# Optimization experiments

Measured on AMD Instinct MI355X. Metric: run time of the kernel, lower is better.

## Reference

```python
import jax, jax.numpy as jnp
import numpy as np

N = 50000      # num nodes
E = 800000     # num edges (before self loops)
F_IN = 128     # fea_size
D = 128        # g_dim_per_layer[i]
H = 4          # heads
C = D // H     # out_channels per head
NEG_SLOPE = 0.2  # PyG GATConv default leaky_relu slope


def setup_inputs() -> dict:
    key = jax.random.key(0)
    ks = jax.random.split(key, 20)
    inp = {
        "x": jax.random.normal(ks[0], (N, F_IN), dtype=jnp.float32),
        "edge_index": jax.random.randint(ks[1], (2, E), 0, N, dtype=jnp.int32),
        "w0": jax.random.normal(ks[2], (F_IN, D), dtype=jnp.float32) * 0.05,
        "b0": jnp.zeros((D,), dtype=jnp.float32),
    }
    for i in (1, 2, 3):
        k = 4 * i
        inp[f"w{i}"] = jax.random.normal(ks[k], (D, D), dtype=jnp.float32) * 0.05
        inp[f"a_src{i}"] = jax.random.normal(ks[k + 1], (H, C), dtype=jnp.float32) * 0.1
        inp[f"a_dst{i}"] = jax.random.normal(ks[k + 2], (H, C), dtype=jnp.float32) * 0.1
        inp[f"b{i}"] = jnp.zeros((D,), dtype=jnp.float32)
    return inp


def _gat_layer(x, src, dst, w, a_src, a_dst, b):
    # PyG GATConv (eval mode, dropout inactive, add_self_loops already applied)
    n = x.shape[0]
    xp = (x @ w).reshape(n, H, C)                       # [N,H,C]
    al_s = jnp.einsum("nhc,hc->nh", xp, a_src)          # [N,H]
    al_d = jnp.einsum("nhc,hc->nh", xp, a_dst)          # [N,H]
    e = jax.nn.leaky_relu(al_s[src] + al_d[dst], NEG_SLOPE)  # [E',H]
    # softmax over incoming edges of each destination node
    m = jax.ops.segment_max(e, dst, num_segments=n)
    e = jnp.exp(e - m[dst])
    s = jax.ops.segment_sum(e, dst, num_segments=n)
    alpha = e / s[dst]                                  # [E',H]
    msg = alpha[:, :, None] * xp[src]                   # [E',H,C]
    out = jax.ops.segment_sum(msg, dst, num_segments=n)  # [N,H,C]
    return out.reshape(n, H * C) + b


def reference(x, edge_index, w0, b0, w1, a_src1, a_dst1, b1,
              w2, a_src2, a_dst2, b2, w3, a_src3, a_dst3, b3):
    n = x.shape[0]
    loops = jnp.arange(n, dtype=edge_index.dtype)
    ei = jnp.concatenate([edge_index, jnp.stack([loops, loops])], axis=1)
    src, dst = ei[0], ei[1]  # messages flow src -> dst (PyG convention)

    h = x @ w0 + b0
    h = jax.nn.relu(h + _gat_layer(h, src, dst, w1, a_src1, a_dst1, b1))
    h = jax.nn.relu(h + _gat_layer(h, src, dst, w2, a_src2, a_dst2, b2))
    return _gat_layer(h, src, dst, w3, a_src3, a_dst3, b3)
```

## Files before the change

### kernel.cpp

```cpp
#include <hip/hip_runtime.h>

#define F 128
#define HEADS 4
#define NEG 0.2f
#define CAP 64
#define CAPP 68
#define CB 6144

typedef unsigned short u16;
typedef unsigned int u32;
typedef __attribute__((ext_vector_type(8))) unsigned short us8;
typedef __attribute__((ext_vector_type(8))) short short8;
typedef __attribute__((ext_vector_type(4))) float f32x4;

__device__ __forceinline__ float bf2f(u16 u) {
  union { u32 i; float f; } v; v.i = ((u32)u) << 16; return v.f;
}
__device__ __forceinline__ float bflo(u32 p) {
  union { u32 i; float f; } v; v.i = p << 16; return v.f;
}
__device__ __forceinline__ float bfhi(u32 p) {
  union { u32 i; float f; } v; v.i = p & 0xFFFF0000u; return v.f;
}
__device__ __forceinline__ u16 f2bf(float f) {
  union { u32 i; float f; } v; v.f = f;
  if (((v.i >> 23) & 0xFF) == 0xFF) return 0;
  u32 r = v.i + 0x7FFF + ((v.i >> 16) & 1);
  return (u16)(r >> 16);
}
__device__ __forceinline__ float sane(float f) {
  union { u32 i; float f; } v; v.f = f;
  return (((v.i >> 23) & 0xFF) == 0xFF) ? 0.f : f;
}
__device__ __forceinline__ u16 bfsane(u16 u) {
  return (((u >> 7) & 0xFF) == 0xFF) ? (u16)0 : u;
}

__device__ __forceinline__ bool detect_f32_wave(const u16* __restrict__ p) {
  int lane = threadIdx.x & 63;
  const us8* q = (const us8*)p + lane * 4;
  int c = 0;
  #pragma unroll
  for (int k = 0; k < 4; k++) {
    us8 v = q[k];
    #pragma unroll
    for (int j = 0; j < 8; j++) { unsigned e = (v[j] >> 7) & 0xFF; c += (e >= 0xF8); }
  }
  #pragma unroll
  for (int off = 32; off; off >>= 1) c += __shfl_xor(c, off);
  return c > 4;
}

__global__ __launch_bounds__(256) void fill_const_bf16(u16* __restrict__ p, u16 v, int n) {
  int i = blockIdx.x * blockDim.x + threadIdx.x;
  if (i < n) p[i] = v;
}

__global__ __launch_bounds__(256) void setup(
    const void* w0, const void* w1, const void* w2, const void* w3,
    const void* b0, const void* b1, const void* b2, const void* b3,
    const void* as1, const void* ad1, const void* as2, const void* ad2,
    const void* as3, const void* ad3,
    u16* __restrict__ wsz, u16* __restrict__ avf, float* __restrict__ par,
    int* __restrict__ flg, int* __restrict__ gcur) {
  __shared__ float vv[8][128];
  bool f32 = detect_f32_wave((const u16*)w0);
  int blk = blockIdx.x, tid = threadIdx.x;
  if (blk < 32) {
    int idx = blk * 256 + tid;
    int layer = idx >> 11;
    int rest  = idx & 2047;
    int lane = rest & 63;
    int ts   = rest >> 6;
    int s = ts & 3, t = ts >> 2;
    int kbase = s * 32 + (lane >> 4) * 8;
    int nn    = t * 16 + (lane & 15);
    const void* W = (layer == 0) ? w0 : (layer == 1) ? w1 : (layer == 2) ? w2 : w3;
    us8 o;
    #pragma unroll
    for (int j = 0; j < 8; j++) {
      int off = (kbase + j) * F + nn;
      o[j] = f32 ? f2bf(sane(((const float*)W)[off])) : bfsane(((const u16*)W)[off]);
    }
    *(us8*)(wsz + (size_t)idx * 8) = o;
  } else if (blk < 37) {
    int t = (blk - 32) * 256 + tid;
    if (t < 1280) {
      const void* tab[10] = {b0, b1, b2, b3, as1, ad1, as2, ad2, as3, ad3};
      const void* src = tab[t >> 7];
      int idx = t & 127;
      float v = f32 ? ((const float*)src)[idx] : bf2f(((const u16*)src)[idx]);
      par[t] = sane(v);
    }
  } else if (blk == 37) {
    gcur[tid] = 0;
    if (tid == 0) flg[0] = f32 ? 1 : 0;
  } else {
    int l = blk - 38;
    const void* W   = (l == 0) ? w1 : (l == 1) ? w2 : w3;
    const void* asp = (l == 0) ? as1 : (l == 1) ? as2 : as3;
    const void* adp = (l == 0) ? ad1 : (l == 1) ? ad2 : ad3;
    for (int e = tid; e < 1024; e += 256) {
      int vec = e >> 7, k = e & 127;
      int h = vec & 3;
      const void* av = (vec < 4) ? asp : adp;
      float sum = 0.f;
      for (int c = 0; c < 32; c++) {
        int col = h * 32 + c;
        float wv_ = f32 ? ((const float*)W)[k * F + col] : bf2f(((const u16*)W)[k * F + col]);
        float aa  = f32 ? ((const float*)av)[col]        : bf2f(((const u16*)av)[col]);
        sum += sane(wv_) * sane(aa);
      }
      vv[vec][k] = sane(sum);
    }
    __syncthreads();
    int s = tid >> 6, lane = tid & 63;
    int quad = lane >> 4, l15 = lane & 15;
    int kbase = s * 32 + quad * 8;
    us8 o;
    #pragma unroll
    for (int j = 0; j < 8; j++)
      o[j] = (l15 < 8) ? f2bf(vv[l15][kbase + j]) : (u16)0;
    *(us8*)(avf + (((size_t)l * 4 + s) * 64 + lane) * 8) = o;
  }
}

__device__ __forceinline__ void gemm_tile(
    int m0, int lane, const void* __restrict__ A, int f32in,
    const u16* __restrict__ wszL, const float* __restrict__ biasc,
    const u16* __restrict__ avfL, u16* __restrict__ Cm,
    float* __restrict__ al_s, float* __restrict__ al_d, int nrows) {
  int quad = lane >> 4, l15 = lane & 15;
  int mrow = m0 + l15;
  int ml = mrow < nrows ? mrow : (nrows - 1);
  short8 af[4];
  if (f32in) {
    const float* ar = (const float*)A + (size_t)ml * F;
    #pragma unroll
    for (int s = 0; s < 4; s++) {
      float4 u = *(const float4*)(ar + s * 32 + quad * 8);
      float4 v = *(const float4*)(ar + s * 32 + quad * 8 + 4);
      short8 p;
      p[0] = (short)f2bf(sane(u.x)); p[1] = (short)f2bf(sane(u.y));
      p[2] = (short)f2bf(sane(u.z)); p[3] = (short)f2bf(sane(u.w));
      p[4] = (short)f2bf(sane(v.x)); p[5] = (short)f2bf(sane(v.y));
      p[6] = (short)f2bf(sane(v.z)); p[7] = (short)f2bf(sane(v.w));
      af[s] = p;
    }
  } else {
    const u16* ar = (const u16*)A + (size_t)ml * F;
    #pragma unroll
    for (int s = 0; s < 4; s++) af[s] = *(const short8*)(ar + s * 32 + quad * 8);
  }

  f32x4 acc[8];
  #pragma unroll
  for (int t = 0; t < 8; t++) acc[t] = (f32x4){0.f, 0.f, 0.f, 0.f};
  f32x4 accL = (f32x4){0.f, 0.f, 0.f, 0.f};

  #pragma unroll
  for (int s = 0; s < 4; s++) {
    short8 bfr[8];
    #pragma unroll
    for (int t = 0; t < 8; t++)
      bfr[t] = *(const short8*)(wszL + (size_t)(((t << 2) | s) * 64 + lane) * 8);
    if (avfL) {
      short8 av = *(const short8*)(avfL + (size_t)(s * 64 + lane) * 8);
      accL = __builtin_amdgcn_mfma_f32_16x16x32_bf16(af[s], av, accL, 0, 0, 0);
    }
    #pragma unroll
    for (int t = 0; t < 8; t++)
      acc[t] = __builtin_amdgcn_mfma_f32_16x16x32_bf16(af[s], bfr[t], acc[t], 0, 0, 0);
  }

  #pragma unroll
  for (int t = 0; t < 8; t++) {
    int cc = t * 16 + l15;
    float b = biasc ? biasc[cc] : 0.f;
    #pragma unroll
    for (int r = 0; r < 4; r++) {
      int row = m0 + quad * 4 + r;
      if (row < nrows) Cm[(size_t)row * F + cc] = f2bf(sane(acc[t][r] + b));
    }
  }
  if (avfL && l15 < 8) {
    float* dst = (l15 < 4) ? al_s : al_d;
    int h = l15 & 3;
    #pragma unroll
    for (int r = 0; r < 4; r++) {
      int row = m0 + quad * 4 + r;
      if (row < nrows) dst[(size_t)row * 4 + h] = sane(accL[r]);
    }
  }
}

__device__ __forceinline__ void scatter_body(const int* __restrict__ ei,
                                             int* __restrict__ gcur,
                                             int2* __restrict__ ebuf,
                                             int E, int E2, int n, int blk) {
  __shared__ int lcnt[256];
  __shared__ int gbase[256];
  int tid = threadIdx.x;
  lcnt[tid] = 0;
  __syncthreads();
  int srcv[16], dstv[16], rnk[16];
  #pragma unroll
  for (int i = 0; i < 16; i++) {
    int e = blk * 4096 + i * 256 + tid;
    rnk[i] = -1;
    if (e < E2) {
      int src, dst;
      if (e < E) { src = ei[e]; dst = ei[E + e]; }
      else       { src = dst = e - E; }
      if ((unsigned)dst < (unsigned)n) {
        srcv[i] = src; dstv[i] = dst;
        rnk[i] = atomicAdd(&lcnt[dst >> 8], 1);
      }
    }
  }
  __syncthreads();
  int c = lcnt[tid];
  gbase[tid] = c ? atomicAdd(&gcur[tid], c) : 0;
  __syncthreads();
  #pragma unroll
  for (int i = 0; i < 16; i++) {
    if (rnk[i] >= 0) {
      int b = dstv[i] >> 8;
      int slot = gbase[b] + rnk[i];
      if (slot < CB) ebuf[(size_t)b * CB + slot] = make_int2(srcv[i], dstv[i]);
    }
  }
}

__device__ __forceinline__ void fill_body(const int* __restrict__ gcur,
                                          const int2* __restrict__ ebuf,
                                          int* __restrict__ rp,
                                          int* __restrict__ col, int n, int b) {
  __shared__ int sc[256];
  __shared__ int ncnt[256];
  __shared__ int nofs[256];
  __shared__ int wsums[4];
  __shared__ int total_s;
  int tid = threadIdx.x, lane = tid & 63, wv = tid >> 6;
  int v = min(gcur[tid], CB);
  int x = v;
  #pragma unroll
  for (int off = 1; off < 64; off <<= 1) {
    int t = __shfl_up(x, off);
    if (lane >= off) x += t;
  }
  if (lane == 63) wsums[wv] = x;
  __syncthreads();
  int add = 0;
  for (int w = 0; w < wv; w++) add += wsums[w];
  sc[tid] = add + x - v;
  if (tid == 255) total_s = add + x;
  __syncthreads();
  int tot = min(gcur[b], CB);
  int colbase = sc[b];
  const int2* eb = ebuf + (size_t)b * CB;
  ncnt[tid] = 0;
  __syncthreads();
  for (int j = tid; j < tot; j += 256) atomicAdd(&ncnt[eb[j].y & 255], 1);
  __syncthreads();
  v = ncnt[tid];
  x = v;
  #pragma unroll
  for (int off = 1; off < 64; off <<= 1) {
    int t = __shfl_up(x, off);
    if (lane >= off) x += t;
  }
  if (lane == 63) wsums[wv] = x;
  __syncthreads();
  add = 0;
  for (int w = 0; w < wv; w++) add += wsums[w];
  nofs[tid] = add + x - v;
  int node = (b << 8) + tid;
  if (node < n) rp[node] = colbase + nofs[tid];
  if (b == 0 && tid == 0) rp[n] = total_s;
  __syncthreads();
  ncnt[tid] = 0;
  __syncthreads();
  for (int j = tid; j < tot; j += 256) {
    int2 e = eb[j];
    int ln = e.y & 255;
    int r = atomicAdd(&ncnt[ln], 1);
    col[colbase + nofs[ln] + r] = e.x;
  }
}

__global__ __launch_bounds__(256) void scatter_gemm0(
    const int* __restrict__ ei, int* __restrict__ gcur, int2* __restrict__ ebuf,
    int E, int E2, int n, int SB,
    const void* __restrict__ x, const int* __restrict__ flg,
    const u16* __restrict__ wsz, const float* __restrict__ b0c,
    u16* __restrict__ hio) {
  int blk = blockIdx.x;
  if (blk < SB) {
    scatter_body(ei, gcur, ebuf, E, E2, n, blk);
  } else {
    int tid = threadIdx.x, wv = tid >> 6, lane = tid & 63;
    int m0 = (blk - SB) * 64 + wv * 16;
    gemm_tile(m0, lane, x, flg[0], wsz, b0c, nullptr, hio, nullptr, nullptr, n);
  }
}

__global__ __launch_bounds__(256) void fill_gemm1(
    const int* __restrict__ gcur, const int2* __restrict__ ebuf,
    int* __restrict__ rp, int* __restrict__ col, int n, int NBv,
    const void* __restrict__ hA, const u16* __restrict__ wszL,
    const u16* __restrict__ avfL, u16* __restrict__ xp,
    float* __restrict__ al_s, float* __restrict__ al_d) {
  int blk = blockIdx.x;
  if (blk < NBv) {
    fill_body(gcur, ebuf, rp, col, n, blk);
  } else {
    int tid = threadIdx.x, wv = tid >> 6, lane = tid & 63;
    int m0 = (blk - NBv) * 64 + wv * 16;
    gemm_tile(m0, lane, hA, 0, wszL, nullptr, avfL, xp, al_s, al_d, n);
  }
}

__global__ __launch_bounds__(128) void gemm_std(
    const void* __restrict__ A, const u16* __restrict__ wszL,
    const u16* __restrict__ avfL, u16* __restrict__ Cm,
    float* __restrict__ al_s, float* __restrict__ al_d, int nrows) {
  int tid = threadIdx.x, wv = tid >> 6, lane = tid & 63;
  int m0 = blockIdx.x * 32 + wv * 16;
  gemm_tile(m0, lane, A, 0, wszL, nullptr, avfL, Cm, al_s, al_d, nrows);
}

#define ACC8(w_, P_)                                    \
  a0 += (w_) * bflo((P_).x); a1 += (w_) * bfhi((P_).x); \
  a2 += (w_) * bflo((P_).y); a3 += (w_) * bfhi((P_).y); \
  a4 += (w_) * bflo((P_).z); a5 += (w_) * bfhi((P_).z); \
  a6 += (w_) * bflo((P_).w); a7 += (w_) * bfhi((P_).w);

__global__ __launch_bounds__(256) void gat_aggregate(
    const u16* __restrict__ xp, const float* __restrict__ al_s,
    const float* __restrict__ al_d, const int* __restrict__ row_ptr,
    const int* __restrict__ col, const float* __restrict__ biasc,
    u16* __restrict__ hio, const int* __restrict__ flgp,
    int n, int E2, int mode) {
  __shared__ int   sb[4][4][CAP];
  __shared__ float wb[4][4][4][CAPP];
  int tid = threadIdx.x;
  int wv = tid >> 6, lane = tid & 63;
  int q = lane >> 4, g = lane & 15;
  int node = blockIdx.x * 16 + wv * 4 + q;
  bool active = node < n;
  int beg = 0, end = 0;
  float ald_[4] = {0.f, 0.f, 0.f, 0.f};
  if (active) {
    beg = row_ptr[node]; end = row_ptr[node + 1];
    if (beg < 0) beg = 0; if (beg > E2) beg = E2;
    if (end < beg) end = beg; if (end > E2) end = E2;
    float4 qd = ((const float4*)al_d)[node];
    ald_[0] = qd.x; ald_[1] = qd.y; ald_[2] = qd.z; ald_[3] = qd.w;
  }
  int deg = end - beg;
  int ch = g * 8, head = g >> 2;
  u32 cb = (u32)g * 16;
  const char* xpb = (const char*)xp;
  float a0 = 0.f, a1 = 0.f, a2 = 0.f, a3 = 0.f;
  float a4 = 0.f, a5 = 0.f, a6 = 0.f, a7 = 0.f;
  float inv;

  if (deg <= CAP) {
    float er[4][4];
    float m4[4] = {-1e30f, -1e30f, -1e30f, -1e30f};
    #pragma unroll
    for (int it = 0; it < 4; it++) {
      int jj = g + it * 16;
      if (jj < deg) {
        int src = col[beg + jj];
        if ((unsigned)src >= (unsigned)n) src = node;
        sb[wv][q][jj] = src;
        float4 qs = ((const float4*)al_s)[src];
        float as_[4] = {qs.x, qs.y, qs.z, qs.w};
        #pragma unroll
        for (int h = 0; h < 4; h++) {
          float e = as_[h] + ald_[h];
          e = (e > 0.f) ? e : NEG * e;
          er[it][h] = e;
          m4[h] = fmaxf(m4[h], e);
        }
      }
    }
    #pragma unroll
    for (int off = 8; off; off >>= 1)
      #pragma unroll
      for (int h = 0; h < 4; h++) m4[h] = fmaxf(m4[h], __shfl_xor(m4[h], off));
    float s4[4] = {0.f, 0.f, 0.f, 0.f};
    #pragma unroll
    for (int it = 0; it < 4; it++) {
      int jj = g + it * 16;
      if (jj < deg) {
        #pragma unroll
        for (int h = 0; h < 4; h++) {
          float w = __expf(er[it][h] - m4[h]);
          s4[h] += w;
          wb[wv][q][h][jj] = w;
        }
      }
    }
    #pragma unroll
    for (int off = 8; off; off >>= 1)
      #pragma unroll
      for (int h = 0; h < 4; h++) s4[h] += __shfl_xor(s4[h], off);
    inv = (s4[head] > 0.f) ? 1.f / s4[head] : 0.f;
    __asm__ volatile("s_waitcnt lgkmcnt(0)" ::: "memory");
    const int* srow = sb[wv][q];
    const float* wrow = wb[wv][q][head];
    int j = 0;
    if (deg >= 4) {
      int4 sa = *(const int4*)(srow);
      float4 wa = *(const float4*)(wrow);
      uint4 P0 = *(const uint4*)(xpb + (((u32)sa.x << 8) + cb));
      uint4 P1 = *(const uint4*)(xpb + (((u32)sa.y << 8) + cb));
      uint4 P2 = *(const uint4*)(xpb + (((u32)sa.z << 8) + cb));
      uint4 P3 = *(const uint4*)(xpb + (((u32)sa.w << 8) + cb));
      for (; j + 8 <= deg; j += 4) {
        int4 sn = *(const int4*)(srow + j + 4);
        float4 wn = *(const float4*)(wrow + j + 4);
        uint4 Q0 = *(const uint4*)(xpb + (((u32)sn.x << 8) + cb));
        uint4 Q1 = *(const uint4*)(xpb + (((u32)sn.y << 8) + cb));
        uint4 Q2 = *(const uint4*)(xpb + (((u32)sn.z << 8) + cb));
        uint4 Q3 = *(const uint4*)(xpb + (((u32)sn.w << 8) + cb));
        ACC8(wa.x, P0); ACC8(wa.y, P1); ACC8(wa.z, P2); ACC8(wa.w, P3);
        wa = wn; P0 = Q0; P1 = Q1; P2 = Q2; P3 = Q3;
      }
      ACC8(wa.x, P0); ACC8(wa.y, P1); ACC8(wa.z, P2); ACC8(wa.w, P3);
      j += 4;
    }
    for (; j < deg; j++) {
      int s0 = srow[j];
      float w0 = wrow[j];
      uint4 p0 = *(const uint4*)(xpb + (((u32)s0 << 8) + cb));
      ACC8(w0, p0);
    }
    a0 *= inv; a1 *= inv; a2 *= inv; a3 *= inv;
    a4 *= inv; a5 *= inv; a6 *= inv; a7 *= inv;
  } else {
    float m = -1.0e30f, s = 0.f;
    for (int j = beg; j < end; ++j) {
      int src = col[j];
      if ((unsigned)src >= (unsigned)n) continue;
      float e = al_s[src * 4 + head] + ald_[head];
      e = (e > 0.f) ? e : NEG * e;
      float mn = fmaxf(m, e);
      float scale = __expf(m - mn);
      float w = __expf(e - mn);
      uint4 pv = *(const uint4*)(xpb + (((u32)src << 8) + cb));
      s = s * scale + w;
      a0 = a0 * scale + w * bflo(pv.x); a1 = a1 * scale + w * bfhi(pv.x);
      a2 = a2 * scale + w * bflo(pv.y); a3 = a3 * scale + w * bfhi(pv.y);
      a4 = a4 * scale + w * bflo(pv.z); a5 = a5 * scale + w * bfhi(pv.z);
      a6 = a6 * scale + w * bflo(pv.w); a7 = a7 * scale + w * bfhi(pv.w);
      m = mn;
    }
    inv = (s > 0.f) ? 1.f / s : 0.f;
    a0 *= inv; a1 *= inv; a2 *= inv; a3 *= inv;
    a4 *= inv; a5 *= inv; a6 *= inv; a7 *= inv;
  }

  if (!active) return;
  float4 b4a = *(const float4*)(biasc + ch);
  float4 b4b = *(const float4*)(biasc + ch + 4);
  float o0 = sane(a0) + b4a.x, o1 = sane(a1) + b4a.y;
  float o2 = sane(a2) + b4a.z, o3 = sane(a3) + b4a.w;
  float o4 = sane(a4) + b4b.x, o5 = sane(a5) + b4b.y;
  float o6 = sane(a6) + b4b.z, o7 = sane(a7) + b4b.w;
  size_t o = (size_t)node * F + ch;
  if (mode == 0) {
    uint4 hv = *(const uint4*)(hio + o);
    o0 = fmaxf(bflo(hv.x) + o0, 0.f);
    o1 = fmaxf(bfhi(hv.x) + o1, 0.f);
    o2 = fmaxf(bflo(hv.y) + o2, 0.f);
    o3 = fmaxf(bfhi(hv.y) + o3, 0.f);
    o4 = fmaxf(bflo(hv.z) + o4, 0.f);
    o5 = fmaxf(bfhi(hv.z) + o5, 0.f);
    o6 = fmaxf(bflo(hv.w) + o6, 0.f);
    o7 = fmaxf(bfhi(hv.w) + o7, 0.f);
    uint4 st;
    st.x = ((u32)f2bf(sane(o1)) << 16) | (u32)f2bf(sane(o0));
    st.y = ((u32)f2bf(sane(o3)) << 16) | (u32)f2bf(sane(o2));
    st.z = ((u32)f2bf(sane(o5)) << 16) | (u32)f2bf(sane(o4));
    st.w = ((u32)f2bf(sane(o7)) << 16) | (u32)f2bf(sane(o6));
    *(uint4*)(hio + o) = st;
  } else {
    if (flgp[0]) {
      float4 s1 = {sane(o0), sane(o1), sane(o2), sane(o3)};
      float4 s2 = {sane(o4), sane(o5), sane(o6), sane(o7)};
      *(float4*)((float*)hio + o) = s1;
      *(float4*)((float*)hio + o + 4) = s2;
    } else {
      uint4 st;
      st.x = ((u32)f2bf(sane(o1)) << 16) | (u32)f2bf(sane(o0));
      st.y = ((u32)f2bf(sane(o3)) << 16) | (u32)f2bf(sane(o2));
      st.z = ((u32)f2bf(sane(o5)) << 16) | (u32)f2bf(sane(o4));
      st.w = ((u32)f2bf(sane(o7)) << 16) | (u32)f2bf(sane(o6));
      *(uint4*)(hio + o) = st;
    }
  }
}

extern "C" void kernel_launch(void* const* d_in, const int* in_sizes, int n_in,
                              void* d_out, int out_size, void* d_ws, size_t ws_size,
                              hipStream_t stream) {
  const int* ei = (const int*)d_in[1];

  const int N  = in_sizes[0] / F;
  const int E  = in_sizes[1] / 2;
  const int E2 = E + N;
  const int NB = (N + 255) >> 8;
  const int SB = (E2 + 4095) / 4096;
  const int GB64  = (N + 63) / 64;
  const int GB128 = (N + 31) / 32;
  const int AGGB  = (N + 15) / 16;

  uintptr_t base = ((uintptr_t)d_ws + 255) & ~(uintptr_t)255;
  size_t off_par = 0;
  size_t off_flg = off_par + (size_t)1536 * 4;
  size_t off_wsz = off_flg + 256;
  size_t off_avf = off_wsz + (size_t)65536 * 2;
  size_t off_xp  = off_avf + (size_t)6144 * 2;
  size_t off_als = off_xp  + (size_t)N * F * 2;
  size_t off_ald = off_als + (size_t)N * HEADS * 4;
  size_t off_gc  = off_ald + (size_t)N * HEADS * 4;
  size_t off_rp  = off_gc  + 1024;
  size_t off_col = off_rp  + (size_t)(N + 1) * 4;
  size_t off_eb  = (off_col + (size_t)E2 * 4 + 255) & ~(size_t)255;
  size_t need    = off_eb + (size_t)NB * CB * 8 + 512 + ((uintptr_t)d_ws & 255);

  if (ws_size < need) {
    fill_const_bf16<<<(out_size + 255) / 256, 256, 0, stream>>>(
        (u16*)d_out, (u16)0x4316, out_size);
    return;
  }

  float* par   = (float*)(base + off_par);
  int* flg     = (int*)(base + off_flg);
  u16* wsz     = (u16*)(base + off_wsz);
  u16* avf     = (u16*)(base + off_avf);
  u16* xp      = (u16*)(base + off_xp);
  float* al_s  = (float*)(base + off_als);
  float* al_d  = (float*)(base + off_ald);
  int* gcur    = (int*)(base + off_gc);
  int* row_ptr = (int*)(base + off_rp);
  int* col     = (int*)(base + off_col);
  int2* ebuf   = (int2*)(base + off_eb);

  float* bc[4];
  for (int l = 0; l < 4; ++l) bc[l] = par + (size_t)l * 128;

  u16* hio = (u16*)d_out;

  setup<<<41, 256, 0, stream>>>(
      d_in[2], d_in[4], d_in[8], d_in[12],
      d_in[3], d_in[7], d_in[11], d_in[15],
      d_in[5], d_in[6], d_in[9], d_in[10], d_in[13], d_in[14],
      wsz, avf, par, flg, gcur);

  scatter_gemm0<<<SB + GB64, 256, 0, stream>>>(
      ei, gcur, ebuf, E, E2, N, SB, d_in[0], flg, wsz, bc[0], hio);

  fill_gemm1<<<NB + GB64, 256, 0, stream>>>(
      gcur, ebuf, row_ptr, col, N, NB,
      hio, wsz + (size_t)1 * 16384, avf, xp, al_s, al_d);

  gat_aggregate<<<AGGB, 256, 0, stream>>>(
      xp, al_s, al_d, row_ptr, col, bc[1], hio, flg, N, E2, 0);
  gemm_std<<<GB128, 128, 0, stream>>>(hio, wsz + (size_t)2 * 16384,
                                      avf + (size_t)1 * 2048, xp, al_s, al_d, N);
  gat_aggregate<<<AGGB, 256, 0, stream>>>(
      xp, al_s, al_d, row_ptr, col, bc[2], hio, flg, N, E2, 0);
  gemm_std<<<GB128, 128, 0, stream>>>(hio, wsz + (size_t)3 * 16384,
                                      avf + (size_t)2 * 2048, xp, al_s, al_d, N);
  gat_aggregate<<<AGGB, 256, 0, stream>>>(
      xp, al_s, al_d, row_ptr, col, bc[3], hio, flg, N, E2, 1);
}
```

Before: 296.4 us.

## Fuse next-layer GEMM into GAT aggregation kernel with ping-pong buffers

The separate gemm_std launches are removed. Each aggregation block now stages its 16 output rows in shared memory and immediately runs the next layer's MFMA projection and attention-logit products on them. Ping-pong xp/al buffers are added so the fused GEMM can write while other blocks still read the previous projection. This saves two launches and a reread of h, but adds a block-wide sync, extra weight loads per block and more workspace memory.

```diff
diff --git a/kernel.cpp b/kernel.cpp
--- a/kernel.cpp
+++ b/kernel.cpp
@@ -6,6 +6,7 @@
 #define CAP 64
 #define CAPP 68
 #define CB 6144
+#define HTS 136
 
 typedef unsigned short u16;
 typedef unsigned int u32;
@@ -321,29 +322,23 @@
   }
 }
 
-__global__ __launch_bounds__(128) void gemm_std(
-    const void* __restrict__ A, const u16* __restrict__ wszL,
-    const u16* __restrict__ avfL, u16* __restrict__ Cm,
-    float* __restrict__ al_s, float* __restrict__ al_d, int nrows) {
-  int tid = threadIdx.x, wv = tid >> 6, lane = tid & 63;
-  int m0 = blockIdx.x * 32 + wv * 16;
-  gemm_tile(m0, lane, A, 0, wszL, nullptr, avfL, Cm, al_s, al_d, nrows);
-}
-
 #define ACC8(w_, P_)                                    \
   a0 += (w_) * bflo((P_).x); a1 += (w_) * bfhi((P_).x); \
   a2 += (w_) * bflo((P_).y); a3 += (w_) * bfhi((P_).y); \
   a4 += (w_) * bflo((P_).z); a5 += (w_) * bfhi((P_).z); \
   a6 += (w_) * bflo((P_).w); a7 += (w_) * bfhi((P_).w);
 
-__global__ __launch_bounds__(256) void gat_aggregate(
+__global__ __launch_bounds__(256) void gat_agg_gemm(
     const u16* __restrict__ xp, const float* __restrict__ al_s,
     const float* __restrict__ al_d, const int* __restrict__ row_ptr,
     const int* __restrict__ col, const float* __restrict__ biasc,
     u16* __restrict__ hio, const int* __restrict__ flgp,
-    int n, int E2, int mode) {
+    int n, int E2, int mode,
+    const u16* __restrict__ wszL, const u16* __restrict__ avfL,
+    u16* __restrict__ xpo, float* __restrict__ also_, float* __restrict__ aldo) {
   __shared__ int   sb[4][4][CAP];
   __shared__ float wb[4][4][4][CAPP];
+  __shared__ u16   ht[16 * HTS];
   int tid = threadIdx.x;
   int wv = tid >> 6, lane = tid & 63;
   int q = lane >> 4, g = lane & 15;
@@ -464,31 +459,83 @@
     a4 *= inv; a5 *= inv; a6 *= inv; a7 *= inv;
   }
 
-  if (!active) return;
-  float4 b4a = *(const float4*)(biasc + ch);
-  float4 b4b = *(const float4*)(biasc + ch + 4);
-  float o0 = sane(a0) + b4a.x, o1 = sane(a1) + b4a.y;
-  float o2 = sane(a2) + b4a.z, o3 = sane(a3) + b4a.w;
-  float o4 = sane(a4) + b4b.x, o5 = sane(a5) + b4b.y;
-  float o6 = sane(a6) + b4b.z, o7 = sane(a7) + b4b.w;
-  size_t o = (size_t)node * F + ch;
   if (mode == 0) {
-    uint4 hv = *(const uint4*)(hio + o);
-    o0 = fmaxf(bflo(hv.x) + o0, 0.f);
-    o1 = fmaxf(bfhi(hv.x) + o1, 0.f);
-    o2 = fmaxf(bflo(hv.y) + o2, 0.f);
-    o3 = fmaxf(bfhi(hv.y) + o3, 0.f);
-    o4 = fmaxf(bflo(hv.z) + o4, 0.f);
-    o5 = fmaxf(bfhi(hv.z) + o5, 0.f);
-    o6 = fmaxf(bflo(hv.w) + o6, 0.f);
-    o7 = fmaxf(bfhi(hv.w) + o7, 0.f);
-    uint4 st;
-    st.x = ((u32)f2bf(sane(o1)) << 16) | (u32)f2bf(sane(o0));
-    st.y = ((u32)f2bf(sane(o3)) << 16) | (u32)f2bf(sane(o2));
-    st.z = ((u32)f2bf(sane(o5)) << 16) | (u32)f2bf(sane(o4));
-    st.w = ((u32)f2bf(sane(o7)) << 16) | (u32)f2bf(sane(o6));
-    *(uint4*)(hio + o) = st;
+    uint4 st = make_uint4(0u, 0u, 0u, 0u);
+    if (active) {
+      float4 b4a = *(const float4*)(biasc + ch);
+      float4 b4b = *(const float4*)(biasc + ch + 4);
+      float o0 = sane(a0) + b4a.x, o1 = sane(a1) + b4a.y;
+      float o2 = sane(a2) + b4a.z, o3 = sane(a3) + b4a.w;
+      float o4 = sane(a4) + b4b.x, o5 = sane(a5) + b4b.y;
+      float o6 = sane(a6) + b4b.z, o7 = sane(a7) + b4b.w;
+      size_t o = (size_t)node * F + ch;
+      uint4 hv = *(const uint4*)(hio + o);
+      o0 = fmaxf(bflo(hv.x) + o0, 0.f);
+      o1 = fmaxf(bfhi(hv.x) + o1, 0.f);
+      o2 = fmaxf(bflo(hv.y) + o2, 0.f);
+      o3 = fmaxf(bfhi(hv.y) + o3, 0.f);
+      o4 = fmaxf(bflo(hv.z) + o4, 0.f);
+      o5 = fmaxf(bfhi(hv.z) + o5, 0.f);
+      o6 = fmaxf(bflo(hv.w) + o6, 0.f);
+      o7 = fmaxf(bfhi(hv.w) + o7, 0.f);
+      st.x = ((u32)f2bf(sane(o1)) << 16) | (u32)f2bf(sane(o0));
+      st.y = ((u32)f2bf(sane(o3)) << 16) | (u32)f2bf(sane(o2));
+      st.z = ((u32)f2bf(sane(o5)) << 16) | (u32)f2bf(sane(o4));
+      st.w = ((u32)f2bf(sane(o7)) << 16) | (u32)f2bf(sane(o6));
+      *(uint4*)(hio + o) = st;
+    }
+    *(uint4*)&ht[(wv * 4 + q) * HTS + ch] = st;
+    __syncthreads();
+
+    int quad = lane >> 4, l15 = lane & 15;
+    short8 af[4];
+    #pragma unroll
+    for (int s = 0; s < 4; s++)
+      af[s] = *(const short8*)&ht[l15 * HTS + s * 32 + quad * 8];
+    f32x4 acc0 = (f32x4){0.f, 0.f, 0.f, 0.f};
+    f32x4 acc1 = (f32x4){0.f, 0.f, 0.f, 0.f};
+    f32x4 accL = (f32x4){0.f, 0.f, 0.f, 0.f};
+    int t0 = wv * 2;
+    #pragma unroll
+    for (int s = 0; s < 4; s++) {
+      short8 bv0 = *(const short8*)(wszL + (size_t)(((t0 << 2) | s) * 64 + lane) * 8);
+      short8 bv1 = *(const short8*)(wszL + (size_t)((((t0 + 1) << 2) | s) * 64 + lane) * 8);
+      if (wv == 0) {
+        short8 av = *(const short8*)(avfL + (size_t)(s * 64 + lane) * 8);
+        accL = __builtin_amdgcn_mfma_f32_16x16x32_bf16(af[s], av, accL, 0, 0, 0);
+      }
+      acc0 = __builtin_amdgcn_mfma_f32_16x16x32_bf16(af[s], bv0, acc0, 0, 0, 0);
+      acc1 = __builtin_amdgcn_mfma_f32_16x16x32_bf16(af[s], bv1, acc1, 0, 0, 0);
+    }
+    int row0 = blockIdx.x * 16;
+    #pragma unroll
+    for (int tt = 0; tt < 2; tt++) {
+      f32x4 ac = tt ? acc1 : acc0;
+      int cc = (t0 + tt) * 16 + l15;
+      #pragma unroll
+      for (int r = 0; r < 4; r++) {
+        int row = row0 + quad * 4 + r;
+        if (row < n) xpo[(size_t)row * F + cc] = f2bf(sane(ac[r]));
+      }
+    }
+    if (wv == 0 && l15 < 8) {
+      float* dst = (l15 < 4) ? also_ : aldo;
+      int h = l15 & 3;
+      #pragma unroll
+      for (int r = 0; r < 4; r++) {
+        int row = row0 + quad * 4 + r;
+        if (row < n) dst[(size_t)row * 4 + h] = sane(accL[r]);
+      }
+    }
   } else {
+    if (!active) return;
+    float4 b4a = *(const float4*)(biasc + ch);
+    float4 b4b = *(const float4*)(biasc + ch + 4);
+    float o0 = sane(a0) + b4a.x, o1 = sane(a1) + b4a.y;
+    float o2 = sane(a2) + b4a.z, o3 = sane(a3) + b4a.w;
+    float o4 = sane(a4) + b4b.x, o5 = sane(a5) + b4b.y;
+    float o6 = sane(a6) + b4b.z, o7 = sane(a7) + b4b.w;
+    size_t o = (size_t)node * F + ch;
     if (flgp[0]) {
       float4 s1 = {sane(o0), sane(o1), sane(o2), sane(o3)};
       float4 s2 = {sane(o4), sane(o5), sane(o6), sane(o7)};
@@ -516,7 +563,6 @@
   const int NB = (N + 255) >> 8;
   const int SB = (E2 + 4095) / 4096;
   const int GB64  = (N + 63) / 64;
-  const int GB128 = (N + 31) / 32;
   const int AGGB  = (N + 15) / 16;
 
   uintptr_t base = ((uintptr_t)d_ws + 255) & ~(uintptr_t)255;
@@ -531,7 +577,10 @@
   size_t off_rp  = off_gc  + 1024;
   size_t off_col = off_rp  + (size_t)(N + 1) * 4;
   size_t off_eb  = (off_col + (size_t)E2 * 4 + 255) & ~(size_t)255;
-  size_t need    = off_eb + (size_t)NB * CB * 8 + 512 + ((uintptr_t)d_ws & 255);
+  size_t off_xp2 = (off_eb + (size_t)NB * CB * 8 + 255) & ~(size_t)255;
+  size_t off_als2 = off_xp2 + (size_t)N * F * 2;
+  size_t off_ald2 = off_als2 + (size_t)N * HEADS * 4;
+  size_t need    = off_ald2 + (size_t)N * HEADS * 4 + 512 + ((uintptr_t)d_ws & 255);
 
   if (ws_size < need) {
     fill_const_bf16<<<(out_size + 255) / 256, 256, 0, stream>>>(
@@ -543,13 +592,16 @@
   int* flg     = (int*)(base + off_flg);
   u16* wsz     = (u16*)(base + off_wsz);
   u16* avf     = (u16*)(base + off_avf);
-  u16* xp      = (u16*)(base + off_xp);
-  float* al_s  = (float*)(base + off_als);
-  float* al_d  = (float*)(base + off_ald);
+  u16* xpA     = (u16*)(base + off_xp);
+  float* alsA  = (float*)(base + off_als);
+  float* aldA  = (float*)(base + off_ald);
   int* gcur    = (int*)(base + off_gc);
   int* row_ptr = (int*)(base + off_rp);
   int* col     = (int*)(base + off_col);
   int2* ebuf   = (int2*)(base + off_eb);
+  u16* xpB     = (u16*)(base + off_xp2);
+  float* alsB  = (float*)(base + off_als2);
+  float* aldB  = (float*)(base + off_ald2);
 
   float* bc[4];
   for (int l = 0; l < 4; ++l) bc[l] = par + (size_t)l * 128;
@@ -567,16 +619,17 @@
 
   fill_gemm1<<<NB + GB64, 256, 0, stream>>>(
       gcur, ebuf, row_ptr, col, N, NB,
-      hio, wsz + (size_t)1 * 16384, avf, xp, al_s, al_d);
-
-  gat_aggregate<<<AGGB, 256, 0, stream>>>(
-      xp, al_s, al_d, row_ptr, col, bc[1], hio, flg, N, E2, 0);
-  gemm_std<<<GB128, 128, 0, stream>>>(hio, wsz + (size_t)2 * 16384,
-                                      avf + (size_t)1 * 2048, xp, al_s, al_d, N);
-  gat_aggregate<<<AGGB, 256, 0, stream>>>(
-      xp, al_s, al_d, row_ptr, col, bc[2], hio, flg, N, E2, 0);
-  gemm_std<<<GB128, 128, 0, stream>>>(hio, wsz + (size_t)3 * 16384,
-                                      avf + (size_t)2 * 2048, xp, al_s, al_d, N);
-  gat_aggregate<<<AGGB, 256, 0, stream>>>(
-      xp, al_s, al_d, row_ptr, col, bc[3], hio, flg, N, E2, 1);
-}
+      hio, wsz + (size_t)1 * 16384, avf, xpA, alsA, aldA);
+
+  gat_agg_gemm<<<AGGB, 256, 0, stream>>>(
+      xpA, alsA, aldA, row_ptr, col, bc[1], hio, flg, N, E2, 0,
+      wsz + (size_t)2 * 16384, avf + (size_t)1 * 2048, xpB, alsB, aldB);
+
+  gat_agg_gemm<<<AGGB, 256, 0, stream>>>(
+      xpB, alsB, aldB, row_ptr, col, bc[2], hio, flg, N, E2, 0,
+      wsz + (size_t)3 * 16384, avf + (size_t)2 * 2048, xpA, alsA, aldA);
+
+  gat_agg_gemm<<<AGGB, 256, 0, stream>>>(
+      xpA, alsA, aldA, row_ptr, col, bc[3], hio, flg, N, E2, 1,
+      nullptr, nullptr, nullptr, nullptr, nullptr);
+}
```

Measured after the change: 283.0 us. 1.05x faster.
